# Kernel tuning notes

Hardware: AMD Instinct MI355X
Metric: run time of the kernel (lower is better)

Reference implementation:

```python
import math
import jax, jax.numpy as jnp
import numpy as np

B, T, C, H = 4, 2048, 1024, 16
D = C // H  # head dim = 64


def setup_inputs() -> dict:
    key = jax.random.key(0)
    ks = jax.random.split(key, 5)
    s = 1.0 / math.sqrt(C)
    return {
        "x": jax.random.normal(ks[0], (B, T, C), jnp.float32),
        "w_qkv": jax.random.normal(ks[1], (C, 3 * C), jnp.float32) * s,
        "b_qkv": jax.random.normal(ks[2], (3 * C,), jnp.float32) * 0.02,
        "w_out": jax.random.normal(ks[3], (C, C), jnp.float32) * s,
        "b_out": jax.random.normal(ks[4], (C,), jnp.float32) * 0.02,
    }


def reference(x, w_qkv, b_qkv, w_out, b_out):
    # qkv projection: (B,T,C) @ (C,3C) -> split into Q,K,V
    qkv = x @ w_qkv + b_qkv
    q, k, v = jnp.split(qkv, 3, axis=-1)
    # reshape to (B,H,T,D)
    q = q.reshape(B, T, H, D).transpose(0, 2, 1, 3)
    k = k.reshape(B, T, H, D).transpose(0, 2, 1, 3)
    v = v.reshape(B, T, H, D).transpose(0, 2, 1, 3)
    # scaled scores with causal mask
    scores = jnp.einsum("bhqd,bhkd->bhqk", q, k) * (1.0 / math.sqrt(D))
    causal = jnp.tril(jnp.ones((T, T), dtype=bool))
    scores = jnp.where(causal[None, None], scores, -jnp.inf)
    attn = jax.nn.softmax(scores, axis=-1)  # dropout_rate=0 (eval)
    out = jnp.einsum("bhqk,bhkd->bhqd", attn, v)
    out = out.transpose(0, 2, 1, 3).reshape(B, T, C)
    return out @ w_out + b_out
```

## Files before the change

kernel.cpp:

```cpp
#include <hip/hip_runtime.h>
#include <cstdint>
#include <cstddef>

typedef _Float16 h8_t __attribute__((ext_vector_type(8)));
typedef _Float16 h4_t __attribute__((ext_vector_type(4)));
typedef float f32x4 __attribute__((ext_vector_type(4)));
typedef float f32x16 __attribute__((ext_vector_type(16)));
typedef unsigned u32x4 __attribute__((ext_vector_type(4)));

#define MFMA_16x16x32_F16(a, b, c) __builtin_amdgcn_mfma_f32_16x16x32_f16(a, b, c, 0, 0, 0)
#define MFMA_32x32x16_F16(a, b, c) __builtin_amdgcn_mfma_f32_32x32x16_f16(a, b, c, 0, 0, 0)

__device__ inline void gload_lds16(const void* g, void* l) {
  __builtin_amdgcn_global_load_lds((const __attribute__((address_space(1))) void*)g,
                                   (__attribute__((address_space(3))) void*)l, 16, 0, 0);
}

__global__ void cvt_f16_kernel(const float* __restrict__ in, _Float16* __restrict__ out, int n4) {
  int i = blockIdx.x * 256 + threadIdx.x;
  if (i >= n4) return;
  float4 v = reinterpret_cast<const float4*>(in)[i];
  h4_t h;
  h[0] = (_Float16)v.x; h[1] = (_Float16)v.y; h[2] = (_Float16)v.z; h[3] = (_Float16)v.w;
  reinterpret_cast<h4_t*>(out)[i] = h;
}

__global__ void transpose_cvt_kernel(const float* __restrict__ in, _Float16* __restrict__ out,
                                     int R, int Cc) {
  __shared__ float tile[32][33];
  int tx = threadIdx.x & 31;
  int ty = threadIdx.x >> 5;
  int c0 = blockIdx.x * 32;
  int r0 = blockIdx.y * 32;
#pragma unroll
  for (int i = 0; i < 4; ++i)
    tile[ty + i * 8][tx] = in[(size_t)(r0 + ty + i * 8) * Cc + (c0 + tx)];
  __syncthreads();
#pragma unroll
  for (int i = 0; i < 4; ++i)
    out[(size_t)(c0 + ty + i * 8) * R + (r0 + tx)] = (_Float16)tile[tx][ty + i * 8];
}

template <int EPI>
__global__ __launch_bounds__(256, 2) void gemm_bt_kernel(
    const _Float16* __restrict__ A, const _Float16* __restrict__ Bt,
    const float* __restrict__ bias, _Float16* __restrict__ outQ,
    _Float16* __restrict__ outK, _Float16* __restrict__ outV,
    float* __restrict__ outF, int NB) {
  __shared__ _Float16 Al[128 * 32];
  __shared__ _Float16 Bl[128 * 32];
  const int tid = threadIdx.x;
  const int lane = tid & 63;
  const int w = tid >> 6;
  const int bm = blockIdx.x / NB;
  const int bn = blockIdx.x % NB;
  const int wm = w & 1, wn = w >> 1;

  f32x4 acc[4][4] = {};

  const int srow = w * 32 + (lane >> 2);
  const int scol = (lane & 3) * 8;
  const _Float16* Abase = A + (size_t)(bm * 128 + srow) * 1024 + scol;
  const _Float16* Bbase = Bt + (size_t)(bn * 128 + srow) * 1024 + scol;

  for (int kt = 0; kt < 32; ++kt) {
    const int k0 = kt * 32;
#pragma unroll
    for (int c = 0; c < 2; ++c) {
      const int seg = w * 2 + c;
      gload_lds16(Abase + (size_t)(c * 16) * 1024 + k0, &Al[seg * 512 + lane * 8]);
      gload_lds16(Bbase + (size_t)(c * 16) * 1024 + k0, &Bl[seg * 512 + lane * 8]);
    }
    __syncthreads();
    h8_t af[4], bf[4];
#pragma unroll
    for (int i = 0; i < 4; ++i)
      af[i] = *reinterpret_cast<const h8_t*>(&Al[(wm * 64 + i * 16 + (lane & 15)) * 32 + (lane >> 4) * 8]);
#pragma unroll
    for (int j = 0; j < 4; ++j)
      bf[j] = *reinterpret_cast<const h8_t*>(&Bl[(wn * 64 + j * 16 + (lane & 15)) * 32 + (lane >> 4) * 8]);
#pragma unroll
    for (int i = 0; i < 4; ++i)
#pragma unroll
      for (int j = 0; j < 4; ++j)
        acc[i][j] = MFMA_16x16x32_F16(af[i], bf[j], acc[i][j]);
    __syncthreads();
  }

  const int gm0 = bm * 128 + wm * 64;
  const int gn0 = bn * 128 + wn * 64;
#pragma unroll
  for (int i = 0; i < 4; ++i) {
#pragma unroll
    for (int j = 0; j < 4; ++j) {
      const int gn = gn0 + j * 16 + (lane & 15);
      const int tm0 = gm0 + i * 16 + (lane >> 4) * 4;
      const float bv = bias[gn];
      if (EPI == 0) {
        const int which = gn >> 10;
        const int nn = gn & 1023;
        const int h = nn >> 6, d = nn & 63;
        const int t0 = tm0 & 2047, b = tm0 >> 11;
        const int bh = b * 16 + h;
        if (which == 2) {
          h4_t pack;
#pragma unroll
          for (int r = 0; r < 4; ++r) pack[r] = (_Float16)(acc[i][j][r] + bv);
          *reinterpret_cast<h4_t*>(&outV[((size_t)bh * 64 + d) * 2048 + t0]) = pack;
        } else {
          _Float16* dst = (which == 0) ? outQ : outK;
          const float scale = (which == 0) ? 0.18033688011112042f : 1.0f;
#pragma unroll
          for (int r = 0; r < 4; ++r)
            dst[((size_t)bh * 2048 + t0 + r) * 64 + d] = (_Float16)((acc[i][j][r] + bv) * scale);
        }
      } else {
#pragma unroll
        for (int r = 0; r < 4; ++r)
          outF[(size_t)(tm0 + r) * 1024 + gn] = acc[i][j][r] + bv;
      }
    }
  }
}

__device__ inline void stage_kv(const _Float16* __restrict__ Kbh, const _Float16* __restrict__ Vbh,
                                int kt, _Float16* Kd, _Float16* Vd, int w, int lane) {
  const _Float16* Kg = Kbh + (size_t)kt * 64 * 64;
  const _Float16* Vg = Vbh + kt * 64;
#pragma unroll
  for (int c = 0; c < 2; ++c) {
    const int idx = (2 * w + c) * 64 + lane;
    const int row = idx >> 3;
    const int chs = (idx & 7) ^ (row & 7);
    gload_lds16(Kg + row * 64 + chs * 8, Kd + idx * 8);
    gload_lds16(Vg + (size_t)row * 2048 + chs * 8, Vd + idx * 8);
  }
}

__device__ inline void pack_pfrag(const float* e, h8_t* out) {
  unsigned u[8];
#pragma unroll
  for (int i = 0; i < 8; ++i) {
    auto hv = __builtin_amdgcn_cvt_pkrtz(e[2 * i], e[2 * i + 1]);
    u[i] = __builtin_bit_cast(unsigned, hv);
  }
  auto r02 = __builtin_amdgcn_permlane32_swap(u[0], u[2], false, false);
  auto r13 = __builtin_amdgcn_permlane32_swap(u[1], u[3], false, false);
  auto r46 = __builtin_amdgcn_permlane32_swap(u[4], u[6], false, false);
  auto r57 = __builtin_amdgcn_permlane32_swap(u[5], u[7], false, false);
  u32x4 w0 = {(unsigned)r02[0], (unsigned)r13[0], (unsigned)r02[1], (unsigned)r13[1]};
  u32x4 w1 = {(unsigned)r46[0], (unsigned)r57[0], (unsigned)r46[1], (unsigned)r57[1]};
  out[0] = __builtin_bit_cast(h8_t, w0);
  out[1] = __builtin_bit_cast(h8_t, w1);
}

__global__ __launch_bounds__(256, 2) void attn_kernel(
    const _Float16* __restrict__ Q, const _Float16* __restrict__ K,
    const _Float16* __restrict__ Vt, _Float16* __restrict__ O) {
  __shared__ _Float16 Kl[2][64 * 64];
  __shared__ _Float16 Vl[2][64 * 64];
  const int tid = threadIdx.x;
  const int lane = tid & 63;
  const int w = tid >> 6;
  const int hi = lane >> 5;
  const int l31 = lane & 31;
  const int bh = blockIdx.x >> 3;
  const int pr = blockIdx.x & 7;
  const int b = bh >> 4, h = bh & 15;
  const _Float16* Kbh = K + (size_t)bh * 2048 * 64;
  const _Float16* Vbh = Vt + (size_t)bh * 64 * 2048;

#pragma unroll
  for (int gi = 0; gi < 2; ++gi) {
    const int g = gi ? (15 - pr) : pr;
    const int nt = 2 * g + 2;
    const int qbase = g * 128 + w * 32;
    const int qrow = qbase + l31;

    h8_t qf[4];
    const _Float16* Qp = Q + ((size_t)bh * 2048 + qrow) * 64 + hi * 8;
#pragma unroll
    for (int ds = 0; ds < 4; ++ds)
      qf[ds] = *reinterpret_cast<const h8_t*>(Qp + ds * 16);

    f32x16 oa[2] = {};
    float m = -1e30f, lsum = 0.f;

    stage_kv(Kbh, Vbh, 0, &Kl[0][0], &Vl[0][0], w, lane);
    __syncthreads();

    for (int kt = 0; kt < nt; ++kt) {
      const int cur = kt & 1;
      if (kt + 1 < nt)
        stage_kv(Kbh, Vbh, kt + 1, &Kl[cur ^ 1][0], &Vl[cur ^ 1][0], w, lane);

      if (kt * 64 <= qbase + 31) {
        const char* Kb = (const char*)&Kl[cur][0];
        const char* Vb = (const char*)&Vl[cur][0];
        f32x16 s0 = {}, s1 = {};
#pragma unroll
        for (int ds = 0; ds < 4; ++ds) {
          const int bc = ds * 32 + hi * 16;
          h8_t kf0 = *(const h8_t*)(Kb + l31 * 128 + (bc ^ ((l31 & 7) << 4)));
          h8_t kf1 = *(const h8_t*)(Kb + (32 + l31) * 128 + (bc ^ ((l31 & 7) << 4)));
          s0 = MFMA_32x32x16_F16(kf0, qf[ds], s0);
          s1 = MFMA_32x32x16_F16(kf1, qf[ds], s1);
        }
        if (kt >= 2 * g) {
#pragma unroll
          for (int r = 0; r < 16; ++r) {
            const int kr = kt * 64 + (r & 3) + 8 * (r >> 2) + 4 * hi;
            if (kr > qrow) s0[r] = -1e30f;
            if (kr + 32 > qrow) s1[r] = -1e30f;
          }
        }
        float t[16];
#pragma unroll
        for (int r = 0; r < 16; ++r) t[r] = fmaxf(s0[r], s1[r]);
#pragma unroll
        for (int st = 8; st >= 1; st >>= 1)
#pragma unroll
          for (int r = 0; r < st; ++r) t[r] = fmaxf(t[r], t[r + st]);
        const float pmax = fmaxf(t[0], __shfl_xor(t[0], 32));
        const float mnew = fmaxf(m, pmax);
        if (__any(mnew > m + 8.f)) {
          const float al = __builtin_amdgcn_exp2f(m - mnew);
          lsum *= al;
#pragma unroll
          for (int r = 0; r < 16; ++r) { oa[0][r] *= al; oa[1][r] *= al; }
          m = mnew;
        }
        float e0[16], e1[16];
#pragma unroll
        for (int r = 0; r < 16; ++r) {
          e0[r] = __builtin_amdgcn_exp2f(s0[r] - m);
          e1[r] = __builtin_amdgcn_exp2f(s1[r] - m);
        }
        float ps = 0.f;
#pragma unroll
        for (int r = 0; r < 16; ++r) ps += e0[r] + e1[r];
        ps += __shfl_xor(ps, 32);
        lsum += ps;
        h8_t pf[4];
        pack_pfrag(e0, pf + 0);
        pack_pfrag(e1, pf + 2);
#pragma unroll
        for (int dt = 0; dt < 2; ++dt) {
#pragma unroll
          for (int kg = 0; kg < 4; ++kg) {
            const int row = dt * 32 + l31;
            const int bc = kg * 32 + hi * 16;
            h8_t vf = *(const h8_t*)(Vb + row * 128 + (bc ^ ((row & 7) << 4)));
            oa[dt] = MFMA_32x32x16_F16(vf, pf[kg], oa[dt]);
          }
        }
      }
      __syncthreads();
    }

    const float inv = __builtin_amdgcn_rcpf(lsum);
    _Float16* Op = O + ((size_t)b * 2048 + qrow) * 1024 + h * 64;
#pragma unroll
    for (int dt = 0; dt < 2; ++dt) {
#pragma unroll
      for (int rg = 0; rg < 4; ++rg) {
        h4_t pk4;
#pragma unroll
        for (int i = 0; i < 4; ++i) pk4[i] = (_Float16)(oa[dt][rg * 4 + i] * inv);
        *reinterpret_cast<h4_t*>(Op + dt * 32 + rg * 8 + hi * 4) = pk4;
      }
    }
  }
}

extern "C" void kernel_launch(void* const* d_in, const int* in_sizes, int n_in,
                              void* d_out, int out_size, void* d_ws, size_t ws_size,
                              hipStream_t stream) {
  (void)in_sizes; (void)n_in; (void)out_size; (void)ws_size;
  const float* x = (const float*)d_in[0];
  const float* w_qkv = (const float*)d_in[1];
  const float* b_qkv = (const float*)d_in[2];
  const float* w_out = (const float*)d_in[3];
  const float* b_out = (const float*)d_in[4];
  float* out = (float*)d_out;

  char* ws = (char*)d_ws;
  size_t off = 0;
  auto alloc = [&](size_t bytes) {
    void* p = ws + off;
    off += (bytes + 255) & ~(size_t)255;
    return p;
  };
  _Float16* x16 = (_Float16*)alloc((size_t)8192 * 1024 * 2);
  _Float16* wqkvT = (_Float16*)alloc((size_t)3072 * 1024 * 2);
  _Float16* woutT = (_Float16*)alloc((size_t)1024 * 1024 * 2);
  _Float16* Qh = (_Float16*)alloc((size_t)64 * 2048 * 64 * 2);
  _Float16* Kh = (_Float16*)alloc((size_t)64 * 2048 * 64 * 2);
  _Float16* Vth = (_Float16*)alloc((size_t)64 * 64 * 2048 * 2);
  _Float16* Oh = (_Float16*)alloc((size_t)8192 * 1024 * 2);

  cvt_f16_kernel<<<8192, 256, 0, stream>>>(x, x16, 8192 * 1024 / 4);
  transpose_cvt_kernel<<<dim3(3072 / 32, 1024 / 32), 256, 0, stream>>>(w_qkv, wqkvT, 1024, 3072);
  transpose_cvt_kernel<<<dim3(1024 / 32, 1024 / 32), 256, 0, stream>>>(w_out, woutT, 1024, 1024);
  gemm_bt_kernel<0><<<64 * 24, 256, 0, stream>>>(x16, wqkvT, b_qkv, Qh, Kh, Vth, nullptr, 24);
  attn_kernel<<<64 * 8, 256, 0, stream>>>(Qh, Kh, Vth, Oh);
  gemm_bt_kernel<1><<<64 * 8, 256, 0, stream>>>(Oh, woutT, b_out, nullptr, nullptr, nullptr, out, 8);
}
```

Before: 186.5 us.

## Rewrite projection GEMMs with 256-wide tiles, double-buffered LDS and 8-wave ping-pong schedule

Replaces the simple 128x128 single-buffered GEMM with a 512-thread kernel using 256xBN tiles, a K-step of 64, and double-buffered LDS. Global-to-LDS loads for the next stage are interleaved between MFMA quadrants under explicit barriers, waitcnt and setprio. Workgroup indices are remapped for XCD locality. The aim is to hide memory latency and raise MFMA utilisation in the QKV and output projections, at the cost of more registers and LDS per block and lower occupancy.

New measurement: 212.9 us. 1.14x slower.

```diff
diff --git a/kernel.cpp b/kernel.cpp
--- a/kernel.cpp
+++ b/kernel.cpp
@@ -15,6 +15,9 @@
   __builtin_amdgcn_global_load_lds((const __attribute__((address_space(1))) void*)g,
                                    (__attribute__((address_space(3))) void*)l, 16, 0, 0);
 }
+
+#define CFENCE asm volatile("" ::: "memory")
+#define BAR() do { CFENCE; __builtin_amdgcn_s_barrier(); CFENCE; } while (0)
 
 __global__ void cvt_f16_kernel(const float* __restrict__ in, _Float16* __restrict__ out, int n4) {
   int i = blockIdx.x * 256 + threadIdx.x;
@@ -41,83 +44,162 @@
     out[(size_t)(c0 + ty + i * 8) * R + (r0 + tx)] = (_Float16)tile[tx][ty + i * 8];
 }
 
-template <int EPI>
-__global__ __launch_bounds__(256, 2) void gemm_bt_kernel(
+template <int BN, int EPI>
+__global__ __launch_bounds__(512, 2) void gemm8p_kernel(
     const _Float16* __restrict__ A, const _Float16* __restrict__ Bt,
     const float* __restrict__ bias, _Float16* __restrict__ outQ,
     _Float16* __restrict__ outK, _Float16* __restrict__ outV,
     float* __restrict__ outF, int NB) {
-  __shared__ _Float16 Al[128 * 32];
-  __shared__ _Float16 Bl[128 * 32];
+  constexpr int NREP = BN / 64;
+  constexpr int BLOADS = (BN == 256) ? 2 : 1;
+  __shared__ _Float16 Al[2][16384];
+  __shared__ _Float16 Bl[2][BN * 64];
+
   const int tid = threadIdx.x;
   const int lane = tid & 63;
   const int w = tid >> 6;
-  const int bm = blockIdx.x / NB;
-  const int bn = blockIdx.x % NB;
-  const int wm = w & 1, wn = w >> 1;
-
-  f32x4 acc[4][4] = {};
-
-  const int srow = w * 32 + (lane >> 2);
-  const int scol = (lane & 3) * 8;
-  const _Float16* Abase = A + (size_t)(bm * 128 + srow) * 1024 + scol;
-  const _Float16* Bbase = Bt + (size_t)(bn * 128 + srow) * 1024 + scol;
-
-  for (int kt = 0; kt < 32; ++kt) {
-    const int k0 = kt * 32;
-#pragma unroll
-    for (int c = 0; c < 2; ++c) {
-      const int seg = w * 2 + c;
-      gload_lds16(Abase + (size_t)(c * 16) * 1024 + k0, &Al[seg * 512 + lane * 8]);
-      gload_lds16(Bbase + (size_t)(c * 16) * 1024 + k0, &Bl[seg * 512 + lane * 8]);
-    }
-    __syncthreads();
-    h8_t af[4], bf[4];
-#pragma unroll
-    for (int i = 0; i < 4; ++i)
-      af[i] = *reinterpret_cast<const h8_t*>(&Al[(wm * 64 + i * 16 + (lane & 15)) * 32 + (lane >> 4) * 8]);
-#pragma unroll
-    for (int j = 0; j < 4; ++j)
-      bf[j] = *reinterpret_cast<const h8_t*>(&Bl[(wn * 64 + j * 16 + (lane & 15)) * 32 + (lane >> 4) * 8]);
-#pragma unroll
-    for (int i = 0; i < 4; ++i)
-#pragma unroll
-      for (int j = 0; j < 4; ++j)
-        acc[i][j] = MFMA_16x16x32_F16(af[i], bf[j], acc[i][j]);
-    __syncthreads();
-  }
-
-  const int gm0 = bm * 128 + wm * 64;
-  const int gn0 = bn * 128 + wn * 64;
-#pragma unroll
-  for (int i = 0; i < 4; ++i) {
-#pragma unroll
-    for (int j = 0; j < 4; ++j) {
-      const int gn = gn0 + j * 16 + (lane & 15);
-      const int tm0 = gm0 + i * 16 + (lane >> 4) * 4;
+  const int wm = w >> 2, wn = w & 3;
+
+  int wg = blockIdx.x;
+  const int cpx = gridDim.x >> 3;
+  wg = (wg & 7) * cpx + (wg >> 3);
+  const int bm = wg / NB, bn = wg % NB;
+  const int m0 = bm * 256;
+  const int n0 = bn * BN;
+
+  f32x4 acc[8][NREP];
+#pragma unroll
+  for (int m = 0; m < 8; ++m)
+#pragma unroll
+    for (int n = 0; n < NREP; ++n) acc[m][n] = (f32x4){0.f, 0.f, 0.f, 0.f};
+
+  auto stageA = [&](int buf, int k0, int u) {
+#pragma unroll
+    for (int it = 0; it < 2; ++it) {
+      const int s = u * 1024 + it * 512 + tid;
+      gload_lds16(&A[(size_t)(m0 + ((s >> 7) << 4) + (s & 15)) * 1024 +
+                     k0 + ((s >> 6) & 1) * 32 + ((s >> 4) & 3) * 8],
+                  &Al[buf][s * 8]);
+    }
+  };
+  auto stageB = [&](int buf, int k0, int u) {
+#pragma unroll
+    for (int it = 0; it < 2; ++it) {
+      const int s = u * 1024 + it * 512 + tid;
+      gload_lds16(&Bt[(size_t)(n0 + ((s >> 7) << 4) + (s & 15)) * 1024 +
+                      k0 + ((s >> 6) & 1) * 32 + ((s >> 4) & 3) * 8],
+                  &Bl[buf][s * 8]);
+    }
+  };
+
+  stageA(0, 0, 0); stageA(0, 0, 1);
+  stageB(0, 0, 0); if (BLOADS == 2) stageB(0, 0, 1);
+  stageA(1, 64, 0); stageA(1, 64, 1);
+  stageB(1, 64, 0); if (BLOADS == 2) stageB(1, 64, 1);
+  if constexpr (BLOADS == 2) asm volatile("s_waitcnt vmcnt(8)" ::: "memory");
+  else asm volatile("s_waitcnt vmcnt(6)" ::: "memory");
+  BAR();
+
+  h8_t afr[8][2], bfr[NREP][2];
+
+#define QUAD(MH, NLO)                                                        \
+  _Pragma("unroll") for (int m = 0; m < 4; ++m)                              \
+  _Pragma("unroll") for (int n = 0; n < NREP / 2; ++n)                       \
+  _Pragma("unroll") for (int kk = 0; kk < 2; ++kk)                           \
+    acc[(MH)*4 + m][(NLO) + n] =                                             \
+        MFMA_16x16x32_F16(afr[(MH)*4 + m][kk], bfr[(NLO) + n][kk],           \
+                          acc[(MH)*4 + m][(NLO) + n]);
+
+#pragma unroll 1
+  for (int t = 0; t < 16; ++t) {
+    const int buf = t & 1;
+    const int kn = (t + 2) * 64;
+    const bool st = (t + 2) < 16;
+    const _Float16* Ab = &Al[buf][0];
+    const _Float16* Bb = &Bl[buf][0];
+
+#pragma unroll
+    for (int m = 0; m < 8; ++m)
+#pragma unroll
+      for (int kk = 0; kk < 2; ++kk)
+        afr[m][kk] = *(const h8_t*)&Ab[(((wm * 8 + m) * 2 + kk) * 64 + lane) * 8];
+#pragma unroll
+    for (int n = 0; n < NREP / 2; ++n)
+#pragma unroll
+      for (int kk = 0; kk < 2; ++kk)
+        bfr[n][kk] = *(const h8_t*)&Bb[(((wn * NREP + n) * 2 + kk) * 64 + lane) * 8];
+    BAR();
+    asm volatile("s_waitcnt lgkmcnt(0)" ::: "memory");
+    __builtin_amdgcn_sched_barrier(0);
+    __builtin_amdgcn_s_setprio(1);
+    QUAD(0, 0)
+    __builtin_amdgcn_s_setprio(0);
+    BAR();
+
+    if (st) { stageA(buf, kn, 0); stageA(buf, kn, 1); }
+    BAR();
+    __builtin_amdgcn_s_setprio(1);
+    QUAD(1, 0)
+    __builtin_amdgcn_s_setprio(0);
+    BAR();
+
+#pragma unroll
+    for (int n = NREP / 2; n < NREP; ++n)
+#pragma unroll
+      for (int kk = 0; kk < 2; ++kk)
+        bfr[n][kk] = *(const h8_t*)&Bb[(((wn * NREP + n) * 2 + kk) * 64 + lane) * 8];
+    BAR();
+    asm volatile("s_waitcnt lgkmcnt(0)" ::: "memory");
+    __builtin_amdgcn_sched_barrier(0);
+    __builtin_amdgcn_s_setprio(1);
+    QUAD(0, NREP / 2)
+    __builtin_amdgcn_s_setprio(0);
+    BAR();
+
+    if (st) { stageB(buf, kn, 0); if (BLOADS == 2) stageB(buf, kn, 1); }
+    BAR();
+    __builtin_amdgcn_s_setprio(1);
+    QUAD(1, NREP / 2)
+    __builtin_amdgcn_s_setprio(0);
+    if (st) {
+      if constexpr (BLOADS == 2) asm volatile("s_waitcnt vmcnt(8)" ::: "memory");
+      else asm volatile("s_waitcnt vmcnt(6)" ::: "memory");
+    } else {
+      asm volatile("s_waitcnt vmcnt(0)" ::: "memory");
+    }
+    BAR();
+  }
+#undef QUAD
+
+#pragma unroll
+  for (int m = 0; m < 8; ++m) {
+#pragma unroll
+    for (int n = 0; n < NREP; ++n) {
+      const int gn = n0 + wn * (BN / 4) + n * 16 + (lane & 15);
+      const int tm0 = m0 + wm * 128 + m * 16 + (lane >> 4) * 4;
       const float bv = bias[gn];
       if (EPI == 0) {
         const int which = gn >> 10;
         const int nn = gn & 1023;
-        const int h = nn >> 6, d = nn & 63;
+        const int hh = nn >> 6, d = nn & 63;
         const int t0 = tm0 & 2047, b = tm0 >> 11;
-        const int bh = b * 16 + h;
+        const int bh = b * 16 + hh;
         if (which == 2) {
           h4_t pack;
 #pragma unroll
-          for (int r = 0; r < 4; ++r) pack[r] = (_Float16)(acc[i][j][r] + bv);
+          for (int r = 0; r < 4; ++r) pack[r] = (_Float16)(acc[m][n][r] + bv);
           *reinterpret_cast<h4_t*>(&outV[((size_t)bh * 64 + d) * 2048 + t0]) = pack;
         } else {
           _Float16* dst = (which == 0) ? outQ : outK;
           const float scale = (which == 0) ? 0.18033688011112042f : 1.0f;
 #pragma unroll
           for (int r = 0; r < 4; ++r)
-            dst[((size_t)bh * 2048 + t0 + r) * 64 + d] = (_Float16)((acc[i][j][r] + bv) * scale);
+            dst[((size_t)bh * 2048 + t0 + r) * 64 + d] = (_Float16)((acc[m][n][r] + bv) * scale);
         }
       } else {
 #pragma unroll
         for (int r = 0; r < 4; ++r)
-          outF[(size_t)(tm0 + r) * 1024 + gn] = acc[i][j][r] + bv;
+          outF[(size_t)(tm0 + r) * 1024 + gn] = acc[m][n][r] + bv;
       }
     }
   }
@@ -302,7 +384,7 @@
   cvt_f16_kernel<<<8192, 256, 0, stream>>>(x, x16, 8192 * 1024 / 4);
   transpose_cvt_kernel<<<dim3(3072 / 32, 1024 / 32), 256, 0, stream>>>(w_qkv, wqkvT, 1024, 3072);
   transpose_cvt_kernel<<<dim3(1024 / 32, 1024 / 32), 256, 0, stream>>>(w_out, woutT, 1024, 1024);
-  gemm_bt_kernel<0><<<64 * 24, 256, 0, stream>>>(x16, wqkvT, b_qkv, Qh, Kh, Vth, nullptr, 24);
+  gemm8p_kernel<256, 0><<<384, 512, 0, stream>>>(x16, wqkvT, b_qkv, Qh, Kh, Vth, nullptr, 12);
   attn_kernel<<<64 * 8, 256, 0, stream>>>(Qh, Kh, Vth, Oh);
-  gemm_bt_kernel<1><<<64 * 8, 256, 0, stream>>>(Oh, woutT, b_out, nullptr, nullptr, nullptr, out, 8);
-}
+  gemm8p_kernel<128, 1><<<256, 512, 0, stream>>>(Oh, woutT, b_out, nullptr, nullptr, nullptr, out, 8);
+}
```

## Rework GEMM with K=64 tiles, fragment-ordered LDS layout and XCD-aware block remap

Applied to the files above, without the earlier changes.

The 128x128 GEMM now stages a 64-wide K slab per iteration, halving the barrier count. It writes LDS in MFMA-fragment order so each lane reads a contiguous 16 bytes without bank conflicts. Block indices are remapped so consecutive tiles land on the same XCD for better L2 reuse, and launch bounds are raised to 4 waves per SIMD. LDS per block doubles to 32 KB, and the higher occupancy target may limit registers.

After: 215.7 us. +15.7%, slower.

```diff
diff --git a/kernel.cpp b/kernel.cpp
--- a/kernel.cpp
+++ b/kernel.cpp
@@ -42,82 +42,91 @@
 }
 
 template <int EPI>
-__global__ __launch_bounds__(256, 2) void gemm_bt_kernel(
+__global__ __launch_bounds__(256, 4) void gemm128_kernel(
     const _Float16* __restrict__ A, const _Float16* __restrict__ Bt,
     const float* __restrict__ bias, _Float16* __restrict__ outQ,
     _Float16* __restrict__ outK, _Float16* __restrict__ outV,
     float* __restrict__ outF, int NB) {
-  __shared__ _Float16 Al[128 * 32];
-  __shared__ _Float16 Bl[128 * 32];
+  __shared__ _Float16 Al[8192];
+  __shared__ _Float16 Bl[8192];
+
   const int tid = threadIdx.x;
   const int lane = tid & 63;
   const int w = tid >> 6;
-  const int bm = blockIdx.x / NB;
-  const int bn = blockIdx.x % NB;
-  const int wm = w & 1, wn = w >> 1;
-
-  f32x4 acc[4][4] = {};
-
-  const int srow = w * 32 + (lane >> 2);
-  const int scol = (lane & 3) * 8;
-  const _Float16* Abase = A + (size_t)(bm * 128 + srow) * 1024 + scol;
-  const _Float16* Bbase = Bt + (size_t)(bn * 128 + srow) * 1024 + scol;
-
-  for (int kt = 0; kt < 32; ++kt) {
-    const int k0 = kt * 32;
-#pragma unroll
-    for (int c = 0; c < 2; ++c) {
-      const int seg = w * 2 + c;
-      gload_lds16(Abase + (size_t)(c * 16) * 1024 + k0, &Al[seg * 512 + lane * 8]);
-      gload_lds16(Bbase + (size_t)(c * 16) * 1024 + k0, &Bl[seg * 512 + lane * 8]);
+  const int wm = w >> 1, wn = w & 1;
+
+  int wg = blockIdx.x;
+  const int cpx = gridDim.x >> 3;
+  wg = (wg & 7) * cpx + (wg >> 3);
+  const int bm = wg / NB, bn = wg % NB;
+  const int m0 = bm * 128;
+  const int n0 = bn * 128;
+
+  f32x4 acc[4][4];
+#pragma unroll
+  for (int m = 0; m < 4; ++m)
+#pragma unroll
+    for (int n = 0; n < 4; ++n) acc[m][n] = (f32x4){0.f, 0.f, 0.f, 0.f};
+
+#pragma unroll 1
+  for (int t = 0; t < 16; ++t) {
+    const int k0 = t * 64;
+#pragma unroll
+    for (int it = 0; it < 4; ++it) {
+      const int s = it * 256 + tid;
+      const int row = ((s >> 7) << 4) + (s & 15);
+      const int col = ((s >> 6) & 1) * 32 + ((s >> 4) & 3) * 8;
+      gload_lds16(&A[(size_t)(m0 + row) * 1024 + k0 + col], &Al[s * 8]);
+      gload_lds16(&Bt[(size_t)(n0 + row) * 1024 + k0 + col], &Bl[s * 8]);
     }
     __syncthreads();
-    h8_t af[4], bf[4];
-#pragma unroll
-    for (int i = 0; i < 4; ++i)
-      af[i] = *reinterpret_cast<const h8_t*>(&Al[(wm * 64 + i * 16 + (lane & 15)) * 32 + (lane >> 4) * 8]);
-#pragma unroll
-    for (int j = 0; j < 4; ++j)
-      bf[j] = *reinterpret_cast<const h8_t*>(&Bl[(wn * 64 + j * 16 + (lane & 15)) * 32 + (lane >> 4) * 8]);
-#pragma unroll
-    for (int i = 0; i < 4; ++i)
-#pragma unroll
-      for (int j = 0; j < 4; ++j)
-        acc[i][j] = MFMA_16x16x32_F16(af[i], bf[j], acc[i][j]);
+#pragma unroll
+    for (int kk = 0; kk < 2; ++kk) {
+      h8_t af[4], bf[4];
+#pragma unroll
+      for (int mf = 0; mf < 4; ++mf)
+        af[mf] = *(const h8_t*)&Al[(((wm * 4 + mf) * 2 + kk) * 64 + lane) * 8];
+#pragma unroll
+      for (int nf = 0; nf < 4; ++nf)
+        bf[nf] = *(const h8_t*)&Bl[(((wn * 4 + nf) * 2 + kk) * 64 + lane) * 8];
+#pragma unroll
+      for (int mf = 0; mf < 4; ++mf)
+#pragma unroll
+        for (int nf = 0; nf < 4; ++nf)
+          acc[mf][nf] = MFMA_16x16x32_F16(af[mf], bf[nf], acc[mf][nf]);
+    }
     __syncthreads();
   }
 
-  const int gm0 = bm * 128 + wm * 64;
-  const int gn0 = bn * 128 + wn * 64;
-#pragma unroll
-  for (int i = 0; i < 4; ++i) {
-#pragma unroll
-    for (int j = 0; j < 4; ++j) {
-      const int gn = gn0 + j * 16 + (lane & 15);
-      const int tm0 = gm0 + i * 16 + (lane >> 4) * 4;
+#pragma unroll
+  for (int mf = 0; mf < 4; ++mf) {
+#pragma unroll
+    for (int nf = 0; nf < 4; ++nf) {
+      const int gn = n0 + wn * 64 + nf * 16 + (lane & 15);
+      const int tm0 = m0 + wm * 64 + mf * 16 + (lane >> 4) * 4;
       const float bv = bias[gn];
       if (EPI == 0) {
         const int which = gn >> 10;
         const int nn = gn & 1023;
-        const int h = nn >> 6, d = nn & 63;
+        const int hh = nn >> 6, d = nn & 63;
         const int t0 = tm0 & 2047, b = tm0 >> 11;
-        const int bh = b * 16 + h;
+        const int bh = b * 16 + hh;
         if (which == 2) {
           h4_t pack;
 #pragma unroll
-          for (int r = 0; r < 4; ++r) pack[r] = (_Float16)(acc[i][j][r] + bv);
+          for (int r = 0; r < 4; ++r) pack[r] = (_Float16)(acc[mf][nf][r] + bv);
           *reinterpret_cast<h4_t*>(&outV[((size_t)bh * 64 + d) * 2048 + t0]) = pack;
         } else {
           _Float16* dst = (which == 0) ? outQ : outK;
           const float scale = (which == 0) ? 0.18033688011112042f : 1.0f;
 #pragma unroll
           for (int r = 0; r < 4; ++r)
-            dst[((size_t)bh * 2048 + t0 + r) * 64 + d] = (_Float16)((acc[i][j][r] + bv) * scale);
+            dst[((size_t)bh * 2048 + t0 + r) * 64 + d] = (_Float16)((acc[mf][nf][r] + bv) * scale);
         }
       } else {
 #pragma unroll
         for (int r = 0; r < 4; ++r)
-          outF[(size_t)(tm0 + r) * 1024 + gn] = acc[i][j][r] + bv;
+          outF[(size_t)(tm0 + r) * 1024 + gn] = acc[mf][nf][r] + bv;
       }
     }
   }
@@ -302,7 +311,7 @@
   cvt_f16_kernel<<<8192, 256, 0, stream>>>(x, x16, 8192 * 1024 / 4);
   transpose_cvt_kernel<<<dim3(3072 / 32, 1024 / 32), 256, 0, stream>>>(w_qkv, wqkvT, 1024, 3072);
   transpose_cvt_kernel<<<dim3(1024 / 32, 1024 / 32), 256, 0, stream>>>(w_out, woutT, 1024, 1024);
-  gemm_bt_kernel<0><<<64 * 24, 256, 0, stream>>>(x16, wqkvT, b_qkv, Qh, Kh, Vth, nullptr, 24);
+  gemm128_kernel<0><<<64 * 24, 256, 0, stream>>>(x16, wqkvT, b_qkv, Qh, Kh, Vth, nullptr, 24);
   attn_kernel<<<64 * 8, 256, 0, stream>>>(Qh, Kh, Vth, Oh);
-  gemm_bt_kernel<1><<<64 * 8, 256, 0, stream>>>(Oh, woutT, b_out, nullptr, nullptr, nullptr, out, 8);
-}
+  gemm128_kernel<1><<<64 * 8, 256, 0, stream>>>(Oh, woutT, b_out, nullptr, nullptr, nullptr, out, 8);
+}
```

## Double-buffer GEMM LDS tiles and XOR-swizzle chunks to avoid bank conflicts

Applied to the files above, without the earlier changes.

The projection GEMM now uses two LDS buffers for the A and B tiles. The next K tile is issued with global_load_lds while MFMAs run on the current one, so global load latency overlaps compute. It also XOR-swizzles the 16-byte chunk position per row pair, which spreads fragment reads across LDS banks. This doubles LDS use per block and may lower occupancy. Correctness depends on the visible sync placement, since the trailing sync must order buffer reuse.

Result: no change. 185.7 us (-0.4%).

```diff
diff --git a/kernel.cpp b/kernel.cpp
--- a/kernel.cpp
+++ b/kernel.cpp
@@ -47,38 +47,52 @@
     const float* __restrict__ bias, _Float16* __restrict__ outQ,
     _Float16* __restrict__ outK, _Float16* __restrict__ outV,
     float* __restrict__ outF, int NB) {
-  __shared__ _Float16 Al[128 * 32];
-  __shared__ _Float16 Bl[128 * 32];
+  __shared__ _Float16 Al[2][4096];
+  __shared__ _Float16 Bl[2][4096];
   const int tid = threadIdx.x;
   const int lane = tid & 63;
   const int w = tid >> 6;
   const int bm = blockIdx.x / NB;
   const int bn = blockIdx.x % NB;
   const int wm = w & 1, wn = w >> 1;
-
-  f32x4 acc[4][4] = {};
-
-  const int srow = w * 32 + (lane >> 2);
-  const int scol = (lane & 3) * 8;
-  const _Float16* Abase = A + (size_t)(bm * 128 + srow) * 1024 + scol;
-  const _Float16* Bbase = Bt + (size_t)(bn * 128 + srow) * 1024 + scol;
-
-  for (int kt = 0; kt < 32; ++kt) {
+  const int m0 = bm * 128, n0 = bn * 128;
+
+  f32x4 acc[4][4];
+#pragma unroll
+  for (int m = 0; m < 4; ++m)
+#pragma unroll
+    for (int n = 0; n < 4; ++n) acc[m][n] = (f32x4){0.f, 0.f, 0.f, 0.f};
+
+  auto stage = [&](int buf, int kt) {
     const int k0 = kt * 32;
 #pragma unroll
     for (int c = 0; c < 2; ++c) {
       const int seg = w * 2 + c;
-      gload_lds16(Abase + (size_t)(c * 16) * 1024 + k0, &Al[seg * 512 + lane * 8]);
-      gload_lds16(Bbase + (size_t)(c * 16) * 1024 + k0, &Bl[seg * 512 + lane * 8]);
-    }
-    __syncthreads();
+      const int row = seg * 16 + (lane >> 2);
+      const int chunk = (lane & 3) ^ ((row >> 1) & 3);
+      gload_lds16(&A[(size_t)(m0 + row) * 1024 + k0 + chunk * 8], &Al[buf][seg * 512 + lane * 8]);
+      gload_lds16(&Bt[(size_t)(n0 + row) * 1024 + k0 + chunk * 8], &Bl[buf][seg * 512 + lane * 8]);
+    }
+  };
+
+  stage(0, 0);
+  __syncthreads();
+
+#pragma unroll 1
+  for (int t = 0; t < 32; ++t) {
+    const int buf = t & 1;
+    if (t + 1 < 32) stage(buf ^ 1, t + 1);
     h8_t af[4], bf[4];
 #pragma unroll
-    for (int i = 0; i < 4; ++i)
-      af[i] = *reinterpret_cast<const h8_t*>(&Al[(wm * 64 + i * 16 + (lane & 15)) * 32 + (lane >> 4) * 8]);
-#pragma unroll
-    for (int j = 0; j < 4; ++j)
-      bf[j] = *reinterpret_cast<const h8_t*>(&Bl[(wn * 64 + j * 16 + (lane & 15)) * 32 + (lane >> 4) * 8]);
+    for (int i = 0; i < 4; ++i) {
+      const int row = wm * 64 + i * 16 + (lane & 15);
+      af[i] = *(const h8_t*)&Al[buf][row * 32 + (((lane >> 4) ^ ((row >> 1) & 3)) * 8)];
+    }
+#pragma unroll
+    for (int j = 0; j < 4; ++j) {
+      const int row = wn * 64 + j * 16 + (lane & 15);
+      bf[j] = *(const h8_t*)&Bl[buf][row * 32 + (((lane >> 4) ^ ((row >> 1) & 3)) * 8)];
+    }
 #pragma unroll
     for (int i = 0; i < 4; ++i)
 #pragma unroll
```
